# Optimization experiments

Hardware: AMD Instinct MI355X
Metric: run time of the kernel (lower is better)

The kernel has to match this reference:

```python
import jax, jax.numpy as jnp
import numpy as np

N, D, F, H, T, R = 8192, 32, 256, 8, 64, 64  # nodes, max neighbors, feats/hidden, heads, time dim, rel dim
HEAD_DIM = F // H
EPS = 1e-5


def _layer_norm(z, g, b):
    mu = jnp.mean(z, axis=-1, keepdims=True)
    var = jnp.mean((z - mu) ** 2, axis=-1, keepdims=True)
    return (z - mu) * jax.lax.rsqrt(var + EPS) * g + b


def _t2v(t, w0, b0, w, b):
    # Time2Vec: first feature linear, rest sinusoidal. t: [...] -> [..., T]
    lin = t[..., None] * w0 + b0                 # [..., 1]
    per = jnp.sin(t[..., None] * w + b)          # [..., T-1]
    return jnp.concatenate([lin, per], axis=-1)


def setup_inputs() -> dict:
    key = jax.random.key(0)
    ks = jax.random.split(key, 12)
    inp = {
        "x": jax.random.normal(ks[0], (N, F), jnp.float32),
        "neighbors": jax.random.randint(ks[1], (N, D), 0, N, dtype=jnp.int32),
        "times": jax.random.uniform(ks[2], (N, D), jnp.float32) * 2.0,
        "rels": jax.random.normal(ks[3], (N, D, R), jnp.float32),
        "kqv_w": jax.random.normal(ks[4], (F, 3 * F), jnp.float32) / np.float32(np.sqrt(F)),
        "t_kqv_w": jax.random.normal(ks[5], (T, 3 * F), jnp.float32) / np.float32(np.sqrt(T)),
        "e_kqv_w": jax.random.normal(ks[6], (R, 3 * F), jnp.float32) / np.float32(np.sqrt(R)),
        "t2v_w0": jax.random.normal(ks[7], (), jnp.float32),
        "t2v_b0": jnp.zeros((), jnp.float32),
        "t2v_w": jax.random.normal(ks[8], (T - 1,), jnp.float32),
        "t2v_b": jnp.zeros((T - 1,), jnp.float32),
        "ln1_g": jnp.ones((F,), jnp.float32),
        "ln1_b": jnp.zeros((F,), jnp.float32),
        "ln2_g": jnp.ones((F,), jnp.float32),
        "ln2_b": jnp.zeros((F,), jnp.float32),
        "lin1_w": jax.random.normal(ks[9], (2 * F, F), jnp.float32) / np.float32(np.sqrt(2 * F)),
        "lin1_b": jnp.zeros((F,), jnp.float32),
        "lin2_w": jax.random.normal(ks[10], (F, F), jnp.float32) / np.float32(np.sqrt(F)),
        "lin2_b": jnp.zeros((F,), jnp.float32),
        "start_t": 0,
        "end_t": 1,
    }
    return inp


def reference(x, neighbors, times, rels, kqv_w, t_kqv_w, e_kqv_w,
              t2v_w0, t2v_b0, t2v_w, t2v_b,
              ln1_g, ln1_b, ln2_g, ln2_b,
              lin1_w, lin1_b, lin2_w, lin2_b,
              start_t, end_t):
    start = jnp.asarray(start_t, jnp.float32)
    end = jnp.asarray(end_t, jnp.float32)

    xn = _layer_norm(x, ln1_g, ln1_b)                       # norm1
    kqv = xn @ kqv_w                                        # [N, 3F]
    k_, q_, v_ = jnp.split(kqv, 3, axis=-1)

    mask = (times >= start) & (times < end)                 # [N, D] valid neighbor edges

    # time-modulation of K/V for each edge (only the needed K and V chunks)
    te = _t2v(times, t2v_w0, t2v_b0, t2v_w, t2v_b)          # [N, D, T]
    t_k = te @ t_kqv_w[:, :F]                               # [N, D, F]
    t_v = te @ t_kqv_w[:, 2 * F:]                           # [N, D, F]
    # query time encoding uses start_t (row 0 in the original cat)
    t_q0 = _t2v(start, t2v_w0, t2v_b0, t2v_w, t2v_b) @ t_kqv_w[:, F:2 * F]  # [F]

    # relation-modulation of K/V
    r_k = rels @ e_kqv_w[:, :F]                             # [N, D, F]
    r_v = rels @ e_kqv_w[:, 2 * F:]                         # [N, D, F]

    k = k_[neighbors] + r_k + t_k                           # [N, D, F] gathered + modulated
    v = v_[neighbors] + r_v + t_v                           # [N, D, F]
    q = q_ + t_q0                                           # [N, F]

    qh = q.reshape(N, H, HEAD_DIM)
    kh = k.reshape(N, D, H, HEAD_DIM)
    vh = v.reshape(N, D, H, HEAD_DIM)

    scale = jnp.float32(1.0 / np.sqrt(HEAD_DIM))
    logits = jnp.einsum('nhd,nmhd->nhm', qh, kh) * scale    # [N, H, D]
    logits = jnp.where(mask[:, None, :], logits, jnp.float32(-1e9))
    attn = jax.nn.softmax(logits, axis=-1)                  # softmax over neighbors
    out = jnp.einsum('nhm,nmhd->nhd', attn, vh).reshape(N, F)
    has_nbr = mask.any(axis=1)                              # empty neighborhood -> zeros
    out = jnp.where(has_nbr[:, None], out, jnp.float32(0.0))

    h2 = out + xn                                           # residual on normed x
    hn = _layer_norm(h2, ln2_g, ln2_b)                      # norm2
    h = jnp.concatenate([xn, hn], axis=1)                   # [N, 2F]
    h = jax.nn.relu(h @ lin1_w + lin1_b) @ lin2_w + lin2_b
    return h + h2
```

## Files before the change

kernel.cpp:

```cpp
#include <hip/hip_runtime.h>
#include <math.h>

#define NN 8192
#define DD 32
#define FF 256
#define HH 8
#define TT 64
#define RR 64

constexpr size_t OFF_KQV  = 0;
constexpr size_t OFF_WQT  = 6*1024*1024;
constexpr size_t OFF_WQE  = 10*1024*1024;
constexpr size_t OFF_H2   = 14*1024*1024;
constexpr size_t OFF_TQ0  = 16*1024*1024;
constexpr size_t OFF_HN   = 0;
constexpr size_t OFF_MID  = 2*1024*1024;
constexpr size_t WS_NEED_FLOATS = 16*1024*1024 + 256;

static __device__ __forceinline__ float scalar_in_f(const void* p) {
    int iv = *(const int*)p;
    unsigned u = (unsigned)iv;
    if (u < 256u) return (float)iv;
    return __int_as_float(iv);
}

__global__ __launch_bounds__(256) void k_layernorm(
    const float* __restrict__ X, const float* __restrict__ g,
    const float* __restrict__ b, float* __restrict__ Y) {
    int w = threadIdx.x >> 6, lane = threadIdx.x & 63;
    int row = blockIdx.x * 4 + w;
    const float* xr = X + (size_t)row * FF;
    float4 v = *(const float4*)(xr + lane * 4);
    float s  = v.x + v.y + v.z + v.w;
    float s2 = v.x*v.x + v.y*v.y + v.z*v.z + v.w*v.w;
#pragma unroll
    for (int m = 32; m >= 1; m >>= 1) {
        s  += __shfl_xor(s, m);
        s2 += __shfl_xor(s2, m);
    }
    float mu  = s * (1.f/FF);
    float var = fmaxf(s2 * (1.f/FF) - mu*mu, 0.f);
    float rs  = rsqrtf(var + 1e-5f);
    float4 gv = *(const float4*)(g + lane*4);
    float4 bv = *(const float4*)(b + lane*4);
    float4 o;
    o.x = (v.x - mu) * rs * gv.x + bv.x;
    o.y = (v.y - mu) * rs * gv.y + bv.y;
    o.z = (v.z - mu) * rs * gv.z + bv.z;
    o.w = (v.w - mu) * rs * gv.w + bv.w;
    *(float4*)(Y + (size_t)row * FF + lane*4) = o;
}

__global__ __launch_bounds__(256) void k_gemm128(
    const float* __restrict__ A0, const float* __restrict__ A1,
    const float* __restrict__ Bp, int ldb,
    const float* __restrict__ bias, const float* __restrict__ resid,
    float* __restrict__ C, int Nn, int K, int doRelu) {
    __shared__ float As[32][132];
    __shared__ float Bs[32][128];
    int m0 = blockIdx.x * 128, n0 = blockIdx.y * 128;
    int tx = threadIdx.x & 15, ty = threadIdx.x >> 4;
    float acc[8][8] = {};
    int nkt = K >> 5;
    for (int kt = 0; kt < nkt; ++kt) {
        int k0 = kt << 5;
        const float* Abase = (k0 < 256) ? A0 : A1;
        int kbase = (k0 < 256) ? k0 : (k0 - 256);
#pragma unroll
        for (int i = 0; i < 4; ++i) {
            int row = (threadIdx.x >> 3) + i*32;
            int kk  = (threadIdx.x & 7) * 4;
            float4 v = *(const float4*)(Abase + (size_t)(m0 + row)*256 + kbase + kk);
            As[kk+0][row] = v.x; As[kk+1][row] = v.y;
            As[kk+2][row] = v.z; As[kk+3][row] = v.w;
        }
#pragma unroll
        for (int i = 0; i < 4; ++i) {
            int bk = (threadIdx.x >> 5) + i*8;
            int bn = (threadIdx.x & 31) * 4;
            *(float4*)&Bs[bk][bn] = *(const float4*)(Bp + (size_t)(k0 + bk)*ldb + n0 + bn);
        }
        __syncthreads();
#pragma unroll
        for (int k = 0; k < 32; ++k) {
            float4 a0 = *(const float4*)&As[k][ty*4];
            float4 a1 = *(const float4*)&As[k][64 + ty*4];
            float4 b0 = *(const float4*)&Bs[k][tx*4];
            float4 b1 = *(const float4*)&Bs[k][64 + tx*4];
            float av[8] = {a0.x,a0.y,a0.z,a0.w, a1.x,a1.y,a1.z,a1.w};
            float bv[8] = {b0.x,b0.y,b0.z,b0.w, b1.x,b1.y,b1.z,b1.w};
#pragma unroll
            for (int i = 0; i < 8; ++i)
#pragma unroll
                for (int j = 0; j < 8; ++j)
                    acc[i][j] = fmaf(av[i], bv[j], acc[i][j]);
        }
        __syncthreads();
    }
    int c0 = n0 + tx*4, c1 = n0 + 64 + tx*4;
    float4 bias0 = {0,0,0,0}, bias1 = {0,0,0,0};
    if (bias) { bias0 = *(const float4*)(bias + c0); bias1 = *(const float4*)(bias + c1); }
#pragma unroll
    for (int i = 0; i < 8; ++i) {
        int ri = m0 + ((i < 4) ? (ty*4 + i) : (64 + ty*4 + i - 4));
        float4 o0 = {acc[i][0]+bias0.x, acc[i][1]+bias0.y, acc[i][2]+bias0.z, acc[i][3]+bias0.w};
        float4 o1 = {acc[i][4]+bias1.x, acc[i][5]+bias1.y, acc[i][6]+bias1.z, acc[i][7]+bias1.w};
        if (doRelu) {
            o0.x=fmaxf(o0.x,0.f); o0.y=fmaxf(o0.y,0.f); o0.z=fmaxf(o0.z,0.f); o0.w=fmaxf(o0.w,0.f);
            o1.x=fmaxf(o1.x,0.f); o1.y=fmaxf(o1.y,0.f); o1.z=fmaxf(o1.z,0.f); o1.w=fmaxf(o1.w,0.f);
        }
        if (resid) {
            float4 r0 = *(const float4*)(resid + (size_t)ri*256 + c0);
            float4 r1 = *(const float4*)(resid + (size_t)ri*256 + c1);
            o0.x+=r0.x; o0.y+=r0.y; o0.z+=r0.z; o0.w+=r0.w;
            o1.x+=r1.x; o1.y+=r1.y; o1.z+=r1.z; o1.w+=r1.w;
        }
        *(float4*)(C + (size_t)ri*Nn + c0) = o0;
        *(float4*)(C + (size_t)ri*Nn + c1) = o1;
    }
}

__global__ __launch_bounds__(256) void k_tq0(
    const float* __restrict__ t2v_w, const float* __restrict__ t2v_b,
    const float* __restrict__ w0p, const float* __restrict__ b0p,
    const void* startp, const float* __restrict__ t_kqv_w,
    float* __restrict__ tq0) {
    __shared__ float te0[64];
    int t = threadIdx.x;
    float start = scalar_in_f(startp);
    if (t < 64)
        te0[t] = (t == 0) ? (start * w0p[0] + b0p[0])
                          : sinf(start * t2v_w[t-1] + t2v_b[t-1]);
    __syncthreads();
    float acc = 0.f;
#pragma unroll 8
    for (int j = 0; j < 64; ++j) acc += te0[j] * t_kqv_w[(size_t)j*768 + 256 + t];
    tq0[t] = acc;
}

__global__ __launch_bounds__(512) void k_wq(
    const float* __restrict__ kqv, const float* __restrict__ tq0,
    const float* __restrict__ t_kqv_w, const float* __restrict__ e_kqv_w,
    float* __restrict__ wqt, float* __restrict__ wqe) {
    __shared__ float qs[16][256];
    int t = threadIdx.x;
    int nb = blockIdx.x * 16;
#pragma unroll
    for (int it = 0; it < 2; ++it) {
        int idx = it*512 + t;
        int g = idx >> 6, c4 = idx & 63;
        float4 q4 = *(const float4*)(kqv + (size_t)(nb+g)*768 + 256 + c4*4);
        float4 t4 = *(const float4*)(tq0 + c4*4);
        q4.x += t4.x; q4.y += t4.y; q4.z += t4.z; q4.w += t4.w;
        *(float4*)&qs[g][c4*4] = q4;
    }
    __syncthreads();
    int j = t & 63, h = t >> 6;
    float4 wt[8], we[8];
#pragma unroll
    for (int cc = 0; cc < 8; ++cc) {
        wt[cc] = *(const float4*)(t_kqv_w + (size_t)j*768 + h*32 + cc*4);
        we[cc] = *(const float4*)(e_kqv_w + (size_t)j*768 + h*32 + cc*4);
    }
    for (int g = 0; g < 16; ++g) {
        float at = 0.f, ae = 0.f;
#pragma unroll
        for (int cc = 0; cc < 8; ++cc) {
            float4 q4 = *(const float4*)&qs[g][h*32 + cc*4];
            at += q4.x*wt[cc].x + q4.y*wt[cc].y + q4.z*wt[cc].z + q4.w*wt[cc].w;
            ae += q4.x*we[cc].x + q4.y*we[cc].y + q4.z*we[cc].z + q4.w*we[cc].w;
        }
        wqt[(size_t)(nb+g)*512 + h*64 + j] = at;
        wqe[(size_t)(nb+g)*512 + h*64 + j] = ae;
    }
}

__global__ __launch_bounds__(256) void k_attn(
    const float* __restrict__ kqv, const float* __restrict__ tq0,
    const float* __restrict__ wqt_g, const float* __restrict__ wqe_g,
    const int* __restrict__ neighbors, const float* __restrict__ times,
    const float* __restrict__ rels,
    const float* __restrict__ t2v_w, const float* __restrict__ t2v_b,
    const float* __restrict__ w0p, const float* __restrict__ b0p,
    const void* startp, const void* endp,
    const float* __restrict__ t_kqv_w, const float* __restrict__ e_kqv_w,
    const float* __restrict__ xn, float* __restrict__ h2) {
    __shared__ __attribute__((aligned(16))) float te[DD][68];
    __shared__ __attribute__((aligned(16))) float wqbuf[2*HH*68];
    __shared__ __attribute__((aligned(16))) float qp[HH][36];
    __shared__ float lg[DD][9];
    __shared__ float at[DD][9];
    __shared__ __attribute__((aligned(16))) float st[HH][68];
    __shared__ __attribute__((aligned(16))) float se[HH][68];
    __shared__ float tms[DD];
    __shared__ int   nbr[DD];
    __shared__ int   msk[DD];

    int n = blockIdx.x;
    int t = threadIdx.x;
    int lane = t & 63, w = t >> 6;
    float startf = scalar_in_f(startp), endf = scalar_in_f(endp);

    if (t < DD) {
        float tv = times[(size_t)n*DD + t];
        tms[t] = tv;
        msk[t] = (tv >= startf && tv < endf) ? 1 : 0;
        nbr[t] = neighbors[(size_t)n*DD + t];
    }
    if (t < 128) {
        int idx = t * 4;
        float4 v = *(const float4*)(wqt_g + (size_t)n*512 + idx);
        *(float4*)&wqbuf[(idx>>6)*68 + (idx&63)] = v;
    } else {
        int idx = (t - 128) * 4;
        float4 v = *(const float4*)(wqe_g + (size_t)n*512 + idx);
        *(float4*)&wqbuf[544 + (idx>>6)*68 + (idx&63)] = v;
    }
    if (t < 64) {
        int f = t * 4;
        float4 q4 = *(const float4*)(kqv + (size_t)n*768 + 256 + f);
        float4 t4 = *(const float4*)(tq0 + f);
        q4.x += t4.x; q4.y += t4.y; q4.z += t4.z; q4.w += t4.w;
        *(float4*)&qp[f>>5][f&31] = q4;
    }
    {
        float wj = (lane == 0) ? 0.f : t2v_w[lane-1];
        float bj = (lane == 0) ? 0.f : t2v_b[lane-1];
        float w0 = w0p[0], b0 = b0p[0];
#pragma unroll
        for (int i = 0; i < 8; ++i) {
            int d2 = w*8 + i;
            float tv = times[(size_t)n*DD + d2];
            te[d2][lane] = (lane == 0) ? fmaf(tv, w0, b0) : __sinf(fmaf(tv, wj, bj));
        }
    }
    __syncthreads();

    int d = t >> 3, h = t & 7;
    float lgv = -1e30f;
    if (msk[d]) {
        const float* rrow   = rels + ((size_t)n*DD + d)*RR;
        const float* wqtrow = &wqbuf[h*68];
        const float* wqerow = &wqbuf[544 + h*68];
        float acc = 0.f;
#pragma unroll
        for (int jc = 0; jc < 16; ++jc) {
            float4 t4 = *(const float4*)&te[d][jc*4];
            float4 a4 = *(const float4*)&wqtrow[jc*4];
            float4 r4 = *(const float4*)(rrow + jc*4);
            float4 e4 = *(const float4*)&wqerow[jc*4];
            acc += t4.x*a4.x + t4.y*a4.y + t4.z*a4.z + t4.w*a4.w
                 + r4.x*e4.x + r4.y*e4.y + r4.z*e4.z + r4.w*e4.w;
        }
        const float* krow = kqv + (size_t)nbr[d]*768 + h*32;
#pragma unroll
        for (int cc = 0; cc < 8; ++cc) {
            float4 k4 = *(const float4*)(krow + cc*4);
            float4 q4 = *(const float4*)&qp[h][cc*4];
            acc += k4.x*q4.x + k4.y*q4.y + k4.z*q4.z + k4.w*q4.w;
        }
        lgv = acc * 0.17677669529663687f;
    }
    lg[d][h] = lgv;
    __syncthreads();

    {
        int dd = t & 31, hh = t >> 5;
        float x = lg[dd][hh];
        float m = x;
#pragma unroll
        for (int mm = 16; mm >= 1; mm >>= 1) m = fmaxf(m, __shfl_xor(m, mm));
        float e = (x > -1e29f) ? __expf(x - m) : 0.f;
        float sden = e;
#pragma unroll
        for (int mm = 16; mm >= 1; mm >>= 1) sden += __shfl_xor(sden, mm);
        at[dd][hh] = (sden > 0.f) ? (e / sden) : 0.f;
    }
    __syncthreads();

    {
        int j = lane, h0 = w, h1 = w + 4;
        const float* rcol = rels + (size_t)n*DD*RR + j;
        float st0 = 0.f, st1 = 0.f, se0 = 0.f, se1 = 0.f;
#pragma unroll 4
        for (int dd = 0; dd < DD; ++dd) {
            float a0 = at[dd][h0], a1 = at[dd][h1];
            float tv = te[dd][j];
            float rv = rcol[(size_t)dd*RR];
            st0 = fmaf(a0, tv, st0); st1 = fmaf(a1, tv, st1);
            se0 = fmaf(a0, rv, se0); se1 = fmaf(a1, rv, se1);
        }
        st[h0][j] = st0; st[h1][j] = st1;
        se[h0][j] = se0; se[h1][j] = se1;
    }

    {
        float4 a4 = {0.f,0.f,0.f,0.f};
        int hh = lane >> 3;
#pragma unroll
        for (int i = 0; i < 8; ++i) {
            int dd = i*4 + w;
            if (msk[dd]) {
                float4 v4 = *(const float4*)(kqv + (size_t)nbr[dd]*768 + 512 + lane*4);
                float a = at[dd][hh];
                a4.x = fmaf(a, v4.x, a4.x); a4.y = fmaf(a, v4.y, a4.y);
                a4.z = fmaf(a, v4.z, a4.z); a4.w = fmaf(a, v4.w, a4.w);
            }
        }
        *(float4*)&wqbuf[w*256 + lane*4] = a4;
    }
    __syncthreads();

    {
        int f = t, hh = f >> 5;
        float og = wqbuf[f] + wqbuf[256 + f] + wqbuf[512 + f] + wqbuf[768 + f];
        float acc = 0.f;
#pragma unroll
        for (int jc = 0; jc < 16; ++jc) {
            float4 s4 = *(const float4*)&st[hh][jc*4];
            float4 e4 = *(const float4*)&se[hh][jc*4];
            acc += s4.x * t_kqv_w[(size_t)(4*jc+0)*768 + 512 + f]
                 + s4.y * t_kqv_w[(size_t)(4*jc+1)*768 + 512 + f]
                 + s4.z * t_kqv_w[(size_t)(4*jc+2)*768 + 512 + f]
                 + s4.w * t_kqv_w[(size_t)(4*jc+3)*768 + 512 + f]
                 + e4.x * e_kqv_w[(size_t)(4*jc+0)*768 + 512 + f]
                 + e4.y * e_kqv_w[(size_t)(4*jc+1)*768 + 512 + f]
                 + e4.z * e_kqv_w[(size_t)(4*jc+2)*768 + 512 + f]
                 + e4.w * e_kqv_w[(size_t)(4*jc+3)*768 + 512 + f];
        }
        size_t o = (size_t)n * FF + f;
        h2[o] = og + acc + xn[o];
    }
}

extern "C" void kernel_launch(void* const* d_in, const int* in_sizes, int n_in,
                              void* d_out, int out_size, void* d_ws, size_t ws_size,
                              hipStream_t stream) {
    (void)in_sizes; (void)n_in;
    const float* x         = (const float*)d_in[0];
    const int*   neighbors = (const int*)d_in[1];
    const float* times     = (const float*)d_in[2];
    const float* rels      = (const float*)d_in[3];
    const float* kqv_w     = (const float*)d_in[4];
    const float* t_kqv_w   = (const float*)d_in[5];
    const float* e_kqv_w   = (const float*)d_in[6];
    const float* t2v_w0    = (const float*)d_in[7];
    const float* t2v_b0    = (const float*)d_in[8];
    const float* t2v_w     = (const float*)d_in[9];
    const float* t2v_b     = (const float*)d_in[10];
    const float* ln1_g     = (const float*)d_in[11];
    const float* ln1_b     = (const float*)d_in[12];
    const float* ln2_g     = (const float*)d_in[13];
    const float* ln2_b     = (const float*)d_in[14];
    const float* lin1_w    = (const float*)d_in[15];
    const float* lin1_b    = (const float*)d_in[16];
    const float* lin2_w    = (const float*)d_in[17];
    const float* lin2_b    = (const float*)d_in[18];
    const void*  startp    = d_in[19];
    const void*  endp      = d_in[20];

    if (ws_size < WS_NEED_FLOATS * sizeof(float)) {
        hipMemsetAsync(d_out, 0, (size_t)out_size * sizeof(float), stream);
        return;
    }

    float* ws   = (float*)d_ws;
    float* kqv  = ws + OFF_KQV;
    float* wqt  = ws + OFF_WQT;
    float* wqe  = ws + OFF_WQE;
    float* h2   = ws + OFF_H2;
    float* tq0  = ws + OFF_TQ0;
    float* hn   = ws + OFF_HN;
    float* mid  = ws + OFF_MID;
    float* out  = (float*)d_out;
    float* xn   = (float*)d_out;

    k_layernorm<<<2048, 256, 0, stream>>>(x, ln1_g, ln1_b, xn);
    k_gemm128<<<dim3(64, 6), 256, 0, stream>>>(xn, nullptr, kqv_w, 768,
                                               nullptr, nullptr, kqv, 768, 256, 0);
    k_tq0<<<1, 256, 0, stream>>>(t2v_w, t2v_b, t2v_w0, t2v_b0, startp, t_kqv_w, tq0);
    k_wq<<<512, 512, 0, stream>>>(kqv, tq0, t_kqv_w, e_kqv_w, wqt, wqe);
    k_attn<<<8192, 256, 0, stream>>>(kqv, tq0, wqt, wqe, neighbors, times, rels,
                                     t2v_w, t2v_b, t2v_w0, t2v_b0, startp, endp,
                                     t_kqv_w, e_kqv_w, xn, h2);
    k_layernorm<<<2048, 256, 0, stream>>>(h2, ln2_g, ln2_b, hn);
    k_gemm128<<<dim3(64, 2), 256, 0, stream>>>(xn, hn, lin1_w, 256,
                                               lin1_b, nullptr, mid, 256, 512, 1);
    k_gemm128<<<dim3(64, 2), 256, 0, stream>>>(mid, nullptr, lin2_w, 256,
                                               lin2_b, h2, out, 256, 256, 0);
}
```

Baseline: 279.6 us.

## Split value projection of attention-weighted time/rel features into separate batched kernel

Each attention block used to project its per-head time and relation summaries through the t_kqv/e_kqv value weights, re-reading 128 weight rows from global memory for every node. The attention kernel now writes those summaries into the wqt/wqe workspace, which it overwrites in place, and stores only the gathered value sum. A new k_vproj kernel keeps the weight columns in registers and processes 16 nodes per block, adding the projection plus the residual. This reuses the weights across nodes at the cost of an extra launch, a global round trip for the summaries and h2, and heavy register use in k_vproj.

```diff
diff --git a/kernel.cpp b/kernel.cpp
--- a/kernel.cpp
+++ b/kernel.cpp
@@ -183,16 +183,13 @@
     const float* __restrict__ t2v_w, const float* __restrict__ t2v_b,
     const float* __restrict__ w0p, const float* __restrict__ b0p,
     const void* startp, const void* endp,
-    const float* __restrict__ t_kqv_w, const float* __restrict__ e_kqv_w,
-    const float* __restrict__ xn, float* __restrict__ h2) {
+    float* __restrict__ st_g, float* __restrict__ se_g,
+    float* __restrict__ h2) {
     __shared__ __attribute__((aligned(16))) float te[DD][68];
     __shared__ __attribute__((aligned(16))) float wqbuf[2*HH*68];
     __shared__ __attribute__((aligned(16))) float qp[HH][36];
     __shared__ float lg[DD][9];
     __shared__ float at[DD][9];
-    __shared__ __attribute__((aligned(16))) float st[HH][68];
-    __shared__ __attribute__((aligned(16))) float se[HH][68];
-    __shared__ float tms[DD];
     __shared__ int   nbr[DD];
     __shared__ int   msk[DD];
 
@@ -203,7 +200,6 @@
 
     if (t < DD) {
         float tv = times[(size_t)n*DD + t];
-        tms[t] = tv;
         msk[t] = (tv >= startf && tv < endf) ? 1 : 0;
         nbr[t] = neighbors[(size_t)n*DD + t];
     }
@@ -290,8 +286,11 @@
             st0 = fmaf(a0, tv, st0); st1 = fmaf(a1, tv, st1);
             se0 = fmaf(a0, rv, se0); se1 = fmaf(a1, rv, se1);
         }
-        st[h0][j] = st0; st[h1][j] = st1;
-        se[h0][j] = se0; se[h1][j] = se1;
+        size_t base = (size_t)n * 512;
+        st_g[base + h0*64 + j] = st0;
+        st_g[base + h1*64 + j] = st1;
+        se_g[base + h0*64 + j] = se0;
+        se_g[base + h1*64 + j] = se1;
     }
 
     {
@@ -312,24 +311,37 @@
     __syncthreads();
 
     {
-        int f = t, hh = f >> 5;
-        float og = wqbuf[f] + wqbuf[256 + f] + wqbuf[512 + f] + wqbuf[768 + f];
+        int f = t;
+        h2[(size_t)n * FF + f] = wqbuf[f] + wqbuf[256 + f] + wqbuf[512 + f] + wqbuf[768 + f];
+    }
+}
+
+__global__ __launch_bounds__(256) void k_vproj(
+    const float* __restrict__ st_g, const float* __restrict__ se_g,
+    const float* __restrict__ t_kqv_w, const float* __restrict__ e_kqv_w,
+    const float* __restrict__ xn, float* __restrict__ h2) {
+    int f = threadIdx.x, h = f >> 5;
+    int nb = blockIdx.x * 16;
+    float wt[64], we[64];
+#pragma unroll
+    for (int j = 0; j < 64; ++j) {
+        wt[j] = t_kqv_w[(size_t)j*768 + 512 + f];
+        we[j] = e_kqv_w[(size_t)j*768 + 512 + f];
+    }
+    for (int g = 0; g < 16; ++g) {
+        int n = nb + g;
+        const float* srow = st_g + (size_t)n*512 + h*64;
+        const float* erow = se_g + (size_t)n*512 + h*64;
         float acc = 0.f;
 #pragma unroll
         for (int jc = 0; jc < 16; ++jc) {
-            float4 s4 = *(const float4*)&st[hh][jc*4];
-            float4 e4 = *(const float4*)&se[hh][jc*4];
-            acc += s4.x * t_kqv_w[(size_t)(4*jc+0)*768 + 512 + f]
-                 + s4.y * t_kqv_w[(size_t)(4*jc+1)*768 + 512 + f]
-                 + s4.z * t_kqv_w[(size_t)(4*jc+2)*768 + 512 + f]
-                 + s4.w * t_kqv_w[(size_t)(4*jc+3)*768 + 512 + f]
-                 + e4.x * e_kqv_w[(size_t)(4*jc+0)*768 + 512 + f]
-                 + e4.y * e_kqv_w[(size_t)(4*jc+1)*768 + 512 + f]
-                 + e4.z * e_kqv_w[(size_t)(4*jc+2)*768 + 512 + f]
-                 + e4.w * e_kqv_w[(size_t)(4*jc+3)*768 + 512 + f];
+            float4 s4 = *(const float4*)(srow + jc*4);
+            float4 e4 = *(const float4*)(erow + jc*4);
+            acc += s4.x*wt[4*jc+0] + s4.y*wt[4*jc+1] + s4.z*wt[4*jc+2] + s4.w*wt[4*jc+3]
+                 + e4.x*we[4*jc+0] + e4.y*we[4*jc+1] + e4.z*we[4*jc+2] + e4.w*we[4*jc+3];
         }
         size_t o = (size_t)n * FF + f;
-        h2[o] = og + acc + xn[o];
+        h2[o] = (h2[o] + acc) + xn[o];
     }
 }
 
@@ -382,7 +394,8 @@
     k_wq<<<512, 512, 0, stream>>>(kqv, tq0, t_kqv_w, e_kqv_w, wqt, wqe);
     k_attn<<<8192, 256, 0, stream>>>(kqv, tq0, wqt, wqe, neighbors, times, rels,
                                      t2v_w, t2v_b, t2v_w0, t2v_b0, startp, endp,
-                                     t_kqv_w, e_kqv_w, xn, h2);
+                                     wqt, wqe, h2);
+    k_vproj<<<512, 256, 0, stream>>>(wqt, wqe, t_kqv_w, e_kqv_w, xn, h2);
     k_layernorm<<<2048, 256, 0, stream>>>(h2, ln2_g, ln2_b, hn);
     k_gemm128<<<dim3(64, 2), 256, 0, stream>>>(xn, hn, lin1_w, 256,
                                                lin1_b, nullptr, mid, 256, 512, 1);
```

After: 319.8 us. +14.4%, slower.
